# Optimization experiments

Measured on AMD Instinct MI355X. Metric: run time of the kernel, lower is better.

The kernel has to match this reference:

```python
import jax, jax.numpy as jnp
import numpy as np

EMBED = 768
N_HEADS = 12
HEAD = EMBED // N_HEADS  # 64
B, T = 2, 2048


def setup_inputs() -> dict:
    key = jax.random.key(0)
    ks = jax.random.split(key, 5)
    s = 0.02
    return {
        "x": jax.random.normal(ks[0], (B, T, EMBED), dtype=jnp.float32),
        "w_attn": jax.random.normal(ks[1], (EMBED, 3 * EMBED), dtype=jnp.float32) * s,
        "b_attn": jnp.zeros((3 * EMBED,), dtype=jnp.float32),
        "w_proj": jax.random.normal(ks[2], (EMBED, EMBED), dtype=jnp.float32) * s,
        "b_proj": jnp.zeros((EMBED,), dtype=jnp.float32),
    }


def reference(x, w_attn, b_attn, w_proj, b_proj):
    b, t, c = x.shape
    scale = HEAD ** -0.5
    qkv = x @ w_attn + b_attn  # [b,t,3c]
    q, k, v = jnp.split(qkv, 3, axis=-1)

    # einops 'b t (h n) -> b n t h' with n=N_HEADS: channel dim factors as
    # (head_size, n_heads) — head index is the inner factor.
    def split_heads(u):
        return u.reshape(b, t, HEAD, N_HEADS).transpose(0, 3, 1, 2)  # [b,n,t,h]

    q, k, v = split_heads(q), split_heads(k), split_heads(v)

    scores = jnp.einsum("bnth,bnsh->bnts", q, k) * scale  # [b,n,t,t]
    causal = jnp.tril(jnp.ones((t, t), dtype=bool))
    scores = jnp.where(causal, scores, jnp.finfo(scores.dtype).min)
    weights = jax.nn.softmax(scores, axis=-1)
    att = jnp.einsum("bnts,bnsh->bnth", weights, v)  # [b,n,t,h]

    # 'b n t h -> b t (n h)': heads are the OUTER factor on output
    att = att.transpose(0, 2, 1, 3).reshape(b, t, c)
    return att @ w_proj + b_proj
```

## Files before the change

### kernel.cpp

```cpp
#include <hip/hip_runtime.h>
#include <hip/hip_bf16.h>
#include <math.h>

#define NB      2
#define T_SZ    2048
#define EMBEDC  768
#define NHEADS  12
#define HEADD   64
#define QKV_PER (NB * NHEADS * T_SZ * HEADD)
#define QSCALE  0.18033688011112042f

typedef __bf16 bf16x8 __attribute__((ext_vector_type(8)));
typedef float  f32x4  __attribute__((ext_vector_type(4)));

__device__ inline ushort f2bf(float x) {
    union { float f; uint u; } v; v.f = x;
    uint r = v.u + 0x7fffu + ((v.u >> 16) & 1u);
    return (ushort)(r >> 16);
}

__device__ inline uint pack2bf(float a, float b) {
    union { __bf16 h[2]; uint u; } t;
    t.h[0] = (__bf16)a; t.h[1] = (__bf16)b;
    return t.u;
}

__device__ inline void gload16(const ushort* g, ushort* l) {
    __builtin_amdgcn_global_load_lds(
        (const __attribute__((address_space(1))) unsigned int*)g,
        (__attribute__((address_space(3))) unsigned int*)l, 16, 0, 0);
}

__global__ __launch_bounds__(256) void cast_k(const float* __restrict__ in,
                                              ushort* __restrict__ out, int n)
{
    int i = (blockIdx.x * 256 + threadIdx.x) * 8;
    if (i >= n) return;
    float4 a = *(const float4*)(in + i);
    float4 b = *(const float4*)(in + i + 4);
    union { ushort u[8]; int4 v; } p;
    p.u[0] = f2bf(a.x); p.u[1] = f2bf(a.y); p.u[2] = f2bf(a.z); p.u[3] = f2bf(a.w);
    p.u[4] = f2bf(b.x); p.u[5] = f2bf(b.y); p.u[6] = f2bf(b.z); p.u[7] = f2bf(b.w);
    *(int4*)(out + i) = p.v;
}

template <int PERM>
__global__ __launch_bounds__(256) void tcast_k(const float* __restrict__ in,
                                               ushort* __restrict__ out,
                                               int R, int C)
{
    __shared__ float t[32][33];
    const int c0 = blockIdx.x * 32, r0 = blockIdx.y * 32;
    const int tx = threadIdx.x & 31, ty = threadIdx.x >> 5;
#pragma unroll
    for (int u = 0; u < 4; ++u)
        t[ty + 8 * u][tx] = in[(size_t)(r0 + ty + 8 * u) * C + c0 + tx];
    __syncthreads();
#pragma unroll
    for (int u = 0; u < 4; ++u) {
        int n = c0 + ty + 8 * u;
        int orow = n;
        if (PERM) {
            int mat = n / EMBEDC, cc = n % EMBEDC;
            orow = mat * EMBEDC + (cc % NHEADS) * HEADD + cc / NHEADS;
        }
        out[(size_t)orow * R + r0 + tx] = f2bf(t[tx][ty + 8 * u]);
    }
}

__global__ __launch_bounds__(256) void vt_k(const ushort* __restrict__ in,
                                            ushort* __restrict__ out)
{
    __shared__ ushort tile[64][66];
    const int bh = blockIdx.y;
    const int t0 = blockIdx.x * 64;
    const int tid = threadIdx.x;
#pragma unroll
    for (int u = 0; u < 2; ++u) {
        int s = tid + 256 * u;
        int r = s >> 3, c8 = s & 7;
        *(bf16x8*)&tile[r][c8 * 8] =
            *(const bf16x8*)(in + ((size_t)bh * T_SZ + t0 + r) * HEADD + c8 * 8);
    }
    __syncthreads();
#pragma unroll
    for (int u = 0; u < 2; ++u) {
        int s = tid + 256 * u;
        int hd = s >> 3, tt = s & 7;
        union { ushort v[8]; int4 q; } pk;
#pragma unroll
        for (int j = 0; j < 8; ++j) pk.v[j] = tile[tt * 8 + j][hd];
        *(int4*)(out + ((size_t)bh * HEADD + hd) * T_SZ + t0 + tt * 8) = pk.q;
    }
}

#define STAGE(buf, koff)                                        \
    do {                                                        \
        gload16(gA0 + (koff), &As[buf][lA0o]);                  \
        gload16(gA1 + (koff), &As[buf][lA1o]);                  \
        gload16(gB0 + (koff), &Bs[buf][lB0o]);                  \
        gload16(gB1 + (koff), &Bs[buf][lB1o]);                  \
    } while (0)

template <int MODE>
__global__ __launch_bounds__(256) void gemm_bf16_k(
    const ushort* __restrict__ A, const ushort* __restrict__ Bt,
    const float* __restrict__ bias, void* __restrict__ outp,
    int M, int N, int K)
{
    __shared__ ushort As[2][128 * 32];
    __shared__ ushort Bs[2][128 * 32];

    const int tid = threadIdx.x;
    const int w = tid >> 6, l = tid & 63;
    const int g = l >> 4, r16 = l & 15;
    const int wr = w >> 1, wc = w & 1;
    const int m0 = blockIdx.y * 128, n0 = blockIdx.x * 128;

    const int srow = l >> 2;
    const int scol = ((l & 3) ^ (srow & 3)) * 8;
    const ushort* gA0 = A + (size_t)(m0 + 32 * w + srow) * K + scol;
    const ushort* gA1 = gA0 + (size_t)16 * K;
    const ushort* gB0 = Bt + (size_t)(n0 + 32 * w + srow) * K + scol;
    const ushort* gB1 = gB0 + (size_t)16 * K;
    const int lA0o = (32 * w) * 32,      lA1o = (32 * w + 16) * 32;
    const int lB0o = lA0o,               lB1o = lA1o;

    f32x4 acc[4][4];
#pragma unroll
    for (int i = 0; i < 4; ++i)
#pragma unroll
        for (int j = 0; j < 4; ++j) acc[i][j] = (f32x4){0.f, 0.f, 0.f, 0.f};

    const int rck = (r16 & 3);

    STAGE(0, 0);
    __syncthreads();

    int cur = 0;
    for (int k0 = 0; k0 < K; k0 += 32) {
        if (k0 + 32 < K) STAGE(cur ^ 1, k0 + 32);

        const ushort* sA = As[cur];
        const ushort* sB = Bs[cur];
        bf16x8 af[4], bfr[4];
#pragma unroll
        for (int ms = 0; ms < 4; ++ms) {
            int row = 64 * wr + 16 * ms + r16;
            af[ms] = *(const bf16x8*)&sA[row * 32 + ((g ^ rck) * 8)];
        }
#pragma unroll
        for (int ns = 0; ns < 4; ++ns) {
            int row = 64 * wc + 16 * ns + r16;
            bfr[ns] = *(const bf16x8*)&sB[row * 32 + ((g ^ rck) * 8)];
        }
#pragma unroll
        for (int ms = 0; ms < 4; ++ms)
#pragma unroll
            for (int ns = 0; ns < 4; ++ns)
                acc[ms][ns] = __builtin_amdgcn_mfma_f32_16x16x32_bf16(
                    af[ms], bfr[ns], acc[ms][ns], 0, 0, 0);

        __syncthreads();
        cur ^= 1;
    }

#pragma unroll
    for (int ns = 0; ns < 4; ++ns) {
        const int n = n0 + 64 * wc + 16 * ns + r16;
        if (MODE == 0) {
            float* out = (float*)outp;
            const float bv = bias[n];
#pragma unroll
            for (int ms = 0; ms < 4; ++ms) {
                const int mb = m0 + 64 * wr + 16 * ms + 4 * g;
#pragma unroll
                for (int r = 0; r < 4; ++r)
                    out[(size_t)(mb + r) * N + n] = acc[ms][ns][r] + bv;
            }
        } else {
            ushort* ob = (ushort*)outp;
            const int mat  = n / EMBEDC;
            const int c    = n - mat * EMBEDC;
            const int head = c >> 6;
            const int hd   = c & 63;
            const float bv = bias[mat * EMBEDC + hd * NHEADS + head];
            const float qs = (mat == 0) ? QSCALE : 1.f;
#pragma unroll
            for (int ms = 0; ms < 4; ++ms) {
                const int mb = m0 + 64 * wr + 16 * ms + 4 * g;
#pragma unroll
                for (int r = 0; r < 4; ++r) {
                    const int m = mb + r;
                    const int b = m >> 11, t = m & 2047;
                    const size_t bh = (size_t)(b * NHEADS + head);
                    ob[(size_t)mat * QKV_PER + (bh * T_SZ + t) * HEADD + hd] =
                        f2bf((acc[ms][ns][r] + bv) * qs);
                }
            }
        }
    }
}

__global__ __launch_bounds__(256, 3) void attn_mfma_k(
    const ushort* __restrict__ Qb, const ushort* __restrict__ Kb,
    const ushort* __restrict__ Vtb, ushort* __restrict__ Out)
{
    __shared__ ushort Ks[128 * 64];
    __shared__ ushort Vs[64 * 128];

    const int qb = blockIdx.x;
    const int bh = blockIdx.y;
    const int bb = bh / NHEADS, head = bh % NHEADS;
    const int tid = threadIdx.x;
    const int w = tid >> 6, l = tid & 63;
    const int g = l >> 4, r16 = l & 15;
    const int q0 = qb * 64;
    const int nt = qb / 2 + 1;
    const ushort* Kg = Qb ? Kb + (size_t)bh * T_SZ * HEADD : nullptr;
    const ushort* Vg = Vtb + (size_t)bh * HEADD * T_SZ;

    bf16x8 qf[2];
    {
        const ushort* qp = Qb + (size_t)bh * T_SZ * HEADD +
                           (size_t)(q0 + 16 * w + r16) * HEADD + g * 8;
        qf[0] = *(const bf16x8*)(qp);
        qf[1] = *(const bf16x8*)(qp + 32);
    }

    f32x4 o[4];
#pragma unroll
    for (int dc = 0; dc < 4; ++dc) o[dc] = (f32x4){0.f, 0.f, 0.f, 0.f};
    float mR = -1e30f, lR = 0.f;

    bf16x8 kr[4], vr[4];
#pragma unroll
    for (int u = 0; u < 4; ++u) {
        int s = tid + 256 * u;
        kr[u] = *(const bf16x8*)(Kg + (size_t)(s >> 3) * HEADD + (s & 7) * 8);
        vr[u] = *(const bf16x8*)(Vg + (size_t)(s >> 4) * T_SZ + (s & 15) * 8);
    }
#pragma unroll
    for (int u = 0; u < 4; ++u) {
        int s = tid + 256 * u;
        int krow = s >> 3, kc8 = s & 7;
        int vrow = s >> 4, vc16 = s & 15;
        *(bf16x8*)&Ks[krow * 64 + ((kc8 ^ (krow & 7)) * 8)] = kr[u];
        *(bf16x8*)&Vs[vrow * 128 + ((vc16 ^ (vrow & 15)) * 8)] = vr[u];
    }
    __syncthreads();

    const int srcLo = ((g & 1) << 5) | r16;
    const int srcHi = srcLo + 16;
    const bool hiSel = (g >> 1) != 0;
    const int qg = q0 + 16 * w + r16;

    for (int kt = 0; kt < nt; ++kt) {
        if (kt + 1 < nt) {
            const int k1 = (kt + 1) * 128;
#pragma unroll
            for (int u = 0; u < 4; ++u) {
                int s = tid + 256 * u;
                kr[u] = *(const bf16x8*)(Kg + (size_t)(k1 + (s >> 3)) * HEADD +
                                         (s & 7) * 8);
                vr[u] = *(const bf16x8*)(Vg + (size_t)(s >> 4) * T_SZ + k1 +
                                         (s & 15) * 8);
            }
        }

        f32x4 st[8];
#pragma unroll
        for (int kc = 0; kc < 8; ++kc) {
            int row = kc * 16 + r16;
            const ushort* krow = &Ks[row * 64];
            bf16x8 a0 = *(const bf16x8*)(krow + ((g    ) ^ (row & 7)) * 8);
            bf16x8 a1 = *(const bf16x8*)(krow + ((g + 4) ^ (row & 7)) * 8);
            f32x4 c = (f32x4){0.f, 0.f, 0.f, 0.f};
            c = __builtin_amdgcn_mfma_f32_16x16x32_bf16(a0, qf[0], c, 0, 0, 0);
            c = __builtin_amdgcn_mfma_f32_16x16x32_bf16(a1, qf[1], c, 0, 0, 0);
            st[kc] = c;
        }

        if (kt == nt - 1) {
            const int k0 = kt * 128;
#pragma unroll
            for (int kc = 0; kc < 8; ++kc)
#pragma unroll
                for (int r = 0; r < 4; ++r)
                    if (k0 + kc * 16 + 4 * g + r > qg) st[kc][r] = -1e30f;
        }

        float pm = -1e30f;
#pragma unroll
        for (int kc = 0; kc < 8; ++kc)
#pragma unroll
            for (int r = 0; r < 4; ++r) pm = fmaxf(pm, st[kc][r]);
        pm = fmaxf(pm, __shfl_xor(pm, 16));
        pm = fmaxf(pm, __shfl_xor(pm, 32));
        if (!__all(pm - mR <= 8.f)) {
            float mNew = fmaxf(mR, pm);
            float sc = exp2f(mR - mNew);
            lR *= sc;
#pragma unroll
            for (int dc = 0; dc < 4; ++dc) o[dc] *= sc;
            mR = mNew;
        }
        float rs = 0.f;
#pragma unroll
        for (int kc = 0; kc < 8; ++kc)
#pragma unroll
            for (int r = 0; r < 4; ++r) {
                float e = exp2f(st[kc][r] - mR);
                st[kc][r] = e;
                rs += e;
            }
        rs += __shfl_xor(rs, 16);
        rs += __shfl_xor(rs, 32);
        lR += rs;

        uint pk[8][2];
#pragma unroll
        for (int kc = 0; kc < 8; ++kc) {
            pk[kc][0] = pack2bf(st[kc][0], st[kc][1]);
            pk[kc][1] = pack2bf(st[kc][2], st[kc][3]);
        }

#pragma unroll
        for (int s = 0; s < 4; ++s) {
            uint A0 = (uint)__shfl((int)pk[2 * s][0],     srcLo);
            uint A1 = (uint)__shfl((int)pk[2 * s][1],     srcLo);
            uint B0 = (uint)__shfl((int)pk[2 * s + 1][0], srcLo);
            uint B1 = (uint)__shfl((int)pk[2 * s + 1][1], srcLo);
            uint A2 = (uint)__shfl((int)pk[2 * s][0],     srcHi);
            uint A3 = (uint)__shfl((int)pk[2 * s][1],     srcHi);
            uint B2 = (uint)__shfl((int)pk[2 * s + 1][0], srcHi);
            uint B3 = (uint)__shfl((int)pk[2 * s + 1][1], srcHi);
            union { uint u[4]; bf16x8 v; } t;
            t.u[0] = hiSel ? B0 : A0;
            t.u[1] = hiSel ? B1 : A1;
            t.u[2] = hiSel ? B2 : A2;
            t.u[3] = hiSel ? B3 : A3;
#pragma unroll
            for (int dc = 0; dc < 4; ++dc) {
                int row = dc * 16 + r16;
                bf16x8 vf = *(const bf16x8*)
                    &Vs[row * 128 + (((4 * s + g) ^ (row & 15)) * 8)];
                o[dc] = __builtin_amdgcn_mfma_f32_16x16x32_bf16(
                    vf, t.v, o[dc], 0, 0, 0);
            }
        }

        __syncthreads();
        if (kt + 1 < nt) {
#pragma unroll
            for (int u = 0; u < 4; ++u) {
                int s = tid + 256 * u;
                int krow = s >> 3, kc8 = s & 7;
                int vrow = s >> 4, vc16 = s & 15;
                *(bf16x8*)&Ks[krow * 64 + ((kc8 ^ (krow & 7)) * 8)] = kr[u];
                *(bf16x8*)&Vs[vrow * 128 + ((vc16 ^ (vrow & 15)) * 8)] = vr[u];
            }
            __syncthreads();
        }
    }

    const float inv = 1.f / lR;
    ushort* orow = Out + ((size_t)(bb * T_SZ + qg)) * EMBEDC + head * HEADD;
#pragma unroll
    for (int dc = 0; dc < 4; ++dc)
#pragma unroll
        for (int r = 0; r < 4; ++r)
            orow[dc * 16 + 4 * g + r] = f2bf(o[dc][r] * inv);
}

extern "C" void kernel_launch(void* const* d_in, const int* in_sizes, int n_in,
                              void* d_out, int out_size, void* d_ws, size_t ws_size,
                              hipStream_t stream)
{
    const float* x      = (const float*)d_in[0];
    const float* w_attn = (const float*)d_in[1];
    const float* b_attn = (const float*)d_in[2];
    const float* w_proj = (const float*)d_in[3];
    const float* b_proj = (const float*)d_in[4];
    float* out = (float*)d_out;

    ushort* qw   = (ushort*)d_ws;
    ushort* vT   = qw + (size_t)3 * QKV_PER;
    ushort* attb = vT + QKV_PER;
    ushort* xb   = attb + QKV_PER;
    ushort* waT  = xb + QKV_PER;
    ushort* wpT  = waT + (size_t)EMBEDC * 3 * EMBEDC;

    cast_k<<<QKV_PER / (256 * 8), 256, 0, stream>>>(x, xb, QKV_PER);
    tcast_k<1><<<dim3(3 * EMBEDC / 32, EMBEDC / 32), 256, 0, stream>>>(
        w_attn, waT, EMBEDC, 3 * EMBEDC);
    tcast_k<0><<<dim3(EMBEDC / 32, EMBEDC / 32), 256, 0, stream>>>(
        w_proj, wpT, EMBEDC, EMBEDC);

    gemm_bf16_k<1><<<dim3(2304 / 128, 4096 / 128), 256, 0, stream>>>(
        xb, waT, b_attn, qw, NB * T_SZ, 3 * EMBEDC, EMBEDC);

    vt_k<<<dim3(T_SZ / 64, NB * NHEADS), 256, 0, stream>>>(
        qw + 2 * (size_t)QKV_PER, vT);

    attn_mfma_k<<<dim3(T_SZ / 64, NB * NHEADS), 256, 0, stream>>>(
        qw, qw + QKV_PER, vT, attb);

    gemm_bf16_k<0><<<dim3(768 / 128, 4096 / 128), 256, 0, stream>>>(
        attb, wpT, b_proj, out, NB * T_SZ, EMBEDC, EMBEDC);
}
```

Before: 131.4 us.

## Split attention KV tile across warps and pair causal query blocks per workgroup

The attention kernel now has each warp process all 64 queries against its own 32-row slice of each 128-key tile, instead of each warp owning 16 queries and sweeping the whole tile. Partial softmax states and outputs are then merged across warps through shared memory. Each workgroup also handles a short and a long causal query block (qb and 31-qb), which halves the grid and balances the triangular work. The cost is more registers (occupancy bound drops from 3 to 2 blocks), extra reduction passes with several barriers, and more LDS.

```diff
diff --git a/kernel.cpp b/kernel.cpp
--- a/kernel.cpp
+++ b/kernel.cpp
@@ -202,175 +202,279 @@
     }
 }
 
-__global__ __launch_bounds__(256, 3) void attn_mfma_k(
+__global__ __launch_bounds__(256, 2) void attn_mfma_k(
     const ushort* __restrict__ Qb, const ushort* __restrict__ Kb,
     const ushort* __restrict__ Vtb, ushort* __restrict__ Out)
 {
-    __shared__ ushort Ks[128 * 64];
-    __shared__ ushort Vs[64 * 128];
-
-    const int qb = blockIdx.x;
+    __shared__ ushort smem[16384];
+    __shared__ float Ml[4 * 64], Ll[4 * 64];
+
+    ushort* Ks = smem;
+    ushort* Vs = smem + 8192;
+
+    const int pairIdx = blockIdx.x;
     const int bh = blockIdx.y;
     const int bb = bh / NHEADS, head = bh % NHEADS;
     const int tid = threadIdx.x;
     const int w = tid >> 6, l = tid & 63;
     const int g = l >> 4, r16 = l & 15;
-    const int q0 = qb * 64;
-    const int nt = qb / 2 + 1;
-    const ushort* Kg = Qb ? Kb + (size_t)bh * T_SZ * HEADD : nullptr;
+    const ushort* Qg = Qb + (size_t)bh * T_SZ * HEADD;
+    const ushort* Kg = Kb + (size_t)bh * T_SZ * HEADD;
     const ushort* Vg = Vtb + (size_t)bh * HEADD * T_SZ;
-
-    bf16x8 qf[2];
-    {
-        const ushort* qp = Qb + (size_t)bh * T_SZ * HEADD +
-                           (size_t)(q0 + 16 * w + r16) * HEADD + g * 8;
-        qf[0] = *(const bf16x8*)(qp);
-        qf[1] = *(const bf16x8*)(qp + 32);
-    }
-
-    f32x4 o[4];
-#pragma unroll
-    for (int dc = 0; dc < 4; ++dc) o[dc] = (f32x4){0.f, 0.f, 0.f, 0.f};
-    float mR = -1e30f, lR = 0.f;
-
-    bf16x8 kr[4], vr[4];
-#pragma unroll
-    for (int u = 0; u < 4; ++u) {
-        int s = tid + 256 * u;
-        kr[u] = *(const bf16x8*)(Kg + (size_t)(s >> 3) * HEADD + (s & 7) * 8);
-        vr[u] = *(const bf16x8*)(Vg + (size_t)(s >> 4) * T_SZ + (s & 15) * 8);
-    }
-#pragma unroll
-    for (int u = 0; u < 4; ++u) {
-        int s = tid + 256 * u;
-        int krow = s >> 3, kc8 = s & 7;
-        int vrow = s >> 4, vc16 = s & 15;
-        *(bf16x8*)&Ks[krow * 64 + ((kc8 ^ (krow & 7)) * 8)] = kr[u];
-        *(bf16x8*)&Vs[vrow * 128 + ((vc16 ^ (vrow & 15)) * 8)] = vr[u];
-    }
-    __syncthreads();
 
     const int srcLo = ((g & 1) << 5) | r16;
     const int srcHi = srcLo + 16;
-    const bool hiSel = (g >> 1) != 0;
-    const int qg = q0 + 16 * w + r16;
-
-    for (int kt = 0; kt < nt; ++kt) {
-        if (kt + 1 < nt) {
-            const int k1 = (kt + 1) * 128;
-#pragma unroll
-            for (int u = 0; u < 4; ++u) {
-                int s = tid + 256 * u;
-                kr[u] = *(const bf16x8*)(Kg + (size_t)(k1 + (s >> 3)) * HEADD +
-                                         (s & 7) * 8);
-                vr[u] = *(const bf16x8*)(Vg + (size_t)(s >> 4) * T_SZ + k1 +
-                                         (s & 15) * 8);
-            }
-        }
-
-        f32x4 st[8];
-#pragma unroll
-        for (int kc = 0; kc < 8; ++kc) {
-            int row = kc * 16 + r16;
-            const ushort* krow = &Ks[row * 64];
-            bf16x8 a0 = *(const bf16x8*)(krow + ((g    ) ^ (row & 7)) * 8);
-            bf16x8 a1 = *(const bf16x8*)(krow + ((g + 4) ^ (row & 7)) * 8);
-            f32x4 c = (f32x4){0.f, 0.f, 0.f, 0.f};
-            c = __builtin_amdgcn_mfma_f32_16x16x32_bf16(a0, qf[0], c, 0, 0, 0);
-            c = __builtin_amdgcn_mfma_f32_16x16x32_bf16(a1, qf[1], c, 0, 0, 0);
-            st[kc] = c;
-        }
-
-        if (kt == nt - 1) {
-            const int k0 = kt * 128;
-#pragma unroll
-            for (int kc = 0; kc < 8; ++kc)
-#pragma unroll
-                for (int r = 0; r < 4; ++r)
-                    if (k0 + kc * 16 + 4 * g + r > qg) st[kc][r] = -1e30f;
-        }
-
-        float pm = -1e30f;
-#pragma unroll
-        for (int kc = 0; kc < 8; ++kc)
-#pragma unroll
-            for (int r = 0; r < 4; ++r) pm = fmaxf(pm, st[kc][r]);
-        pm = fmaxf(pm, __shfl_xor(pm, 16));
-        pm = fmaxf(pm, __shfl_xor(pm, 32));
-        if (!__all(pm - mR <= 8.f)) {
-            float mNew = fmaxf(mR, pm);
-            float sc = exp2f(mR - mNew);
-            lR *= sc;
-#pragma unroll
-            for (int dc = 0; dc < 4; ++dc) o[dc] *= sc;
-            mR = mNew;
-        }
-        float rs = 0.f;
-#pragma unroll
-        for (int kc = 0; kc < 8; ++kc)
-#pragma unroll
-            for (int r = 0; r < 4; ++r) {
-                float e = exp2f(st[kc][r] - mR);
-                st[kc][r] = e;
-                rs += e;
-            }
-        rs += __shfl_xor(rs, 16);
-        rs += __shfl_xor(rs, 32);
-        lR += rs;
-
-        uint pk[8][2];
-#pragma unroll
-        for (int kc = 0; kc < 8; ++kc) {
-            pk[kc][0] = pack2bf(st[kc][0], st[kc][1]);
-            pk[kc][1] = pack2bf(st[kc][2], st[kc][3]);
-        }
-
-#pragma unroll
-        for (int s = 0; s < 4; ++s) {
-            uint A0 = (uint)__shfl((int)pk[2 * s][0],     srcLo);
-            uint A1 = (uint)__shfl((int)pk[2 * s][1],     srcLo);
-            uint B0 = (uint)__shfl((int)pk[2 * s + 1][0], srcLo);
-            uint B1 = (uint)__shfl((int)pk[2 * s + 1][1], srcLo);
-            uint A2 = (uint)__shfl((int)pk[2 * s][0],     srcHi);
-            uint A3 = (uint)__shfl((int)pk[2 * s][1],     srcHi);
-            uint B2 = (uint)__shfl((int)pk[2 * s + 1][0], srcHi);
-            uint B3 = (uint)__shfl((int)pk[2 * s + 1][1], srcHi);
-            union { uint u[4]; bf16x8 v; } t;
-            t.u[0] = hiSel ? B0 : A0;
-            t.u[1] = hiSel ? B1 : A1;
-            t.u[2] = hiSel ? B2 : A2;
-            t.u[3] = hiSel ? B3 : A3;
+    const bool kcSel = (g >> 1) != 0;
+
+    for (int rep = 0; rep < 2; ++rep) {
+        const int qb = rep ? (31 - pairIdx) : pairIdx;
+        const int q0 = qb * 64;
+        const int nt = qb / 2 + 1;
+
+        bf16x8 qf[4][2];
+#pragma unroll
+        for (int qi = 0; qi < 4; ++qi) {
+            const ushort* qp = Qg + (size_t)(q0 + qi * 16 + r16) * HEADD + g * 8;
+            qf[qi][0] = *(const bf16x8*)(qp);
+            qf[qi][1] = *(const bf16x8*)(qp + 32);
+        }
+
+        f32x4 o[4][4];
+#pragma unroll
+        for (int dc = 0; dc < 4; ++dc)
+#pragma unroll
+            for (int qi = 0; qi < 4; ++qi) o[dc][qi] = (f32x4){0.f,0.f,0.f,0.f};
+        float mR[4], lR[4];
+#pragma unroll
+        for (int qi = 0; qi < 4; ++qi) { mR[qi] = -1e30f; lR[qi] = 0.f; }
+
+        __syncthreads();
+
+        bf16x8 kr[4], vr[4];
+#pragma unroll
+        for (int u = 0; u < 4; ++u) {
+            int s = tid + 256 * u;
+            kr[u] = *(const bf16x8*)(Kg + (size_t)(s >> 3) * HEADD + (s & 7) * 8);
+            vr[u] = *(const bf16x8*)(Vg + (size_t)(s >> 4) * T_SZ + (s & 15) * 8);
+        }
+#pragma unroll
+        for (int u = 0; u < 4; ++u) {
+            int s = tid + 256 * u;
+            int krow = s >> 3, kc8 = s & 7;
+            int vrow = s >> 4, vc16 = s & 15;
+            *(bf16x8*)&Ks[krow * 64 + ((kc8 ^ (krow & 7)) * 8)] = kr[u];
+            *(bf16x8*)&Vs[vrow * 128 + ((vc16 ^ (vrow & 15)) * 8)] = vr[u];
+        }
+        __syncthreads();
+
+        for (int kt = 0; kt < nt; ++kt) {
+            if (kt + 1 < nt) {
+                const int k1 = (kt + 1) * 128;
+#pragma unroll
+                for (int u = 0; u < 4; ++u) {
+                    int s = tid + 256 * u;
+                    kr[u] = *(const bf16x8*)(Kg + (size_t)(k1 + (s >> 3)) * HEADD +
+                                             (s & 7) * 8);
+                    vr[u] = *(const bf16x8*)(Vg + (size_t)(s >> 4) * T_SZ + k1 +
+                                             (s & 15) * 8);
+                }
+            }
+
+            f32x4 st[2][4];
+#pragma unroll
+            for (int kc = 0; kc < 2; ++kc) {
+                int row = 32 * w + kc * 16 + r16;
+                const ushort* kp = &Ks[row * 64];
+                bf16x8 a0 = *(const bf16x8*)(kp + ((g    ) ^ (r16 & 7)) * 8);
+                bf16x8 a1 = *(const bf16x8*)(kp + ((g + 4) ^ (r16 & 7)) * 8);
+#pragma unroll
+                for (int qi = 0; qi < 4; ++qi) {
+                    f32x4 c = (f32x4){0.f, 0.f, 0.f, 0.f};
+                    c = __builtin_amdgcn_mfma_f32_16x16x32_bf16(a0, qf[qi][0], c, 0, 0, 0);
+                    c = __builtin_amdgcn_mfma_f32_16x16x32_bf16(a1, qf[qi][1], c, 0, 0, 0);
+                    st[kc][qi] = c;
+                }
+            }
+
+            if (kt == nt - 1) {
+                const int kvb = kt * 128 + 32 * w;
+#pragma unroll
+                for (int kc = 0; kc < 2; ++kc)
+#pragma unroll
+                    for (int qi = 0; qi < 4; ++qi)
+#pragma unroll
+                        for (int r = 0; r < 4; ++r)
+                            if (kvb + kc * 16 + 4 * g + r > q0 + qi * 16 + r16)
+                                st[kc][qi][r] = -1e30f;
+            }
+
+            float pm[4];
+#pragma unroll
+            for (int qi = 0; qi < 4; ++qi) {
+                float m = fmaxf(fmaxf(st[0][qi][0], st[0][qi][1]),
+                                fmaxf(st[0][qi][2], st[0][qi][3]));
+                m = fmaxf(m, fmaxf(fmaxf(st[1][qi][0], st[1][qi][1]),
+                                   fmaxf(st[1][qi][2], st[1][qi][3])));
+                m = fmaxf(m, __shfl_xor(m, 16));
+                m = fmaxf(m, __shfl_xor(m, 32));
+                pm[qi] = m;
+            }
+            float dm = fmaxf(fmaxf(pm[0] - mR[0], pm[1] - mR[1]),
+                             fmaxf(pm[2] - mR[2], pm[3] - mR[3]));
+            if (!__all(dm <= 8.f)) {
+#pragma unroll
+                for (int qi = 0; qi < 4; ++qi) {
+                    float mNew = fmaxf(mR[qi], pm[qi]);
+                    float sc = exp2f(mR[qi] - mNew);
+                    lR[qi] *= sc;
+                    mR[qi] = mNew;
+#pragma unroll
+                    for (int dc = 0; dc < 4; ++dc) o[dc][qi] *= sc;
+                }
+            }
+#pragma unroll
+            for (int qi = 0; qi < 4; ++qi) {
+                float rs = 0.f;
+#pragma unroll
+                for (int kc = 0; kc < 2; ++kc)
+#pragma unroll
+                    for (int r = 0; r < 4; ++r) {
+                        float e = exp2f(st[kc][qi][r] - mR[qi]);
+                        st[kc][qi][r] = e;
+                        rs += e;
+                    }
+                rs += __shfl_xor(rs, 16);
+                rs += __shfl_xor(rs, 32);
+                lR[qi] += rs;
+            }
+
+            uint pk[4][2][2];
+#pragma unroll
+            for (int qi = 0; qi < 4; ++qi)
+#pragma unroll
+                for (int kc = 0; kc < 2; ++kc) {
+                    pk[qi][kc][0] = pack2bf(st[kc][qi][0], st[kc][qi][1]);
+                    pk[qi][kc][1] = pack2bf(st[kc][qi][2], st[kc][qi][3]);
+                }
+
+            bf16x8 vf[4];
 #pragma unroll
             for (int dc = 0; dc < 4; ++dc) {
                 int row = dc * 16 + r16;
-                bf16x8 vf = *(const bf16x8*)
-                    &Vs[row * 128 + (((4 * s + g) ^ (row & 15)) * 8)];
-                o[dc] = __builtin_amdgcn_mfma_f32_16x16x32_bf16(
-                    vf, t.v, o[dc], 0, 0, 0);
-            }
-        }
-
-        __syncthreads();
-        if (kt + 1 < nt) {
-#pragma unroll
-            for (int u = 0; u < 4; ++u) {
-                int s = tid + 256 * u;
-                int krow = s >> 3, kc8 = s & 7;
-                int vrow = s >> 4, vc16 = s & 15;
-                *(bf16x8*)&Ks[krow * 64 + ((kc8 ^ (krow & 7)) * 8)] = kr[u];
-                *(bf16x8*)&Vs[vrow * 128 + ((vc16 ^ (vrow & 15)) * 8)] = vr[u];
-            }
+                vf[dc] = *(const bf16x8*)
+                    &Vs[row * 128 + (((4 * w + g) ^ (row & 15)) * 8)];
+            }
+
+#pragma unroll
+            for (int qi = 0; qi < 4; ++qi) {
+                uint A0 = (uint)__shfl((int)pk[qi][0][0], srcLo);
+                uint A1 = (uint)__shfl((int)pk[qi][0][1], srcLo);
+                uint B0 = (uint)__shfl((int)pk[qi][1][0], srcLo);
+                uint B1 = (uint)__shfl((int)pk[qi][1][1], srcLo);
+                uint A2 = (uint)__shfl((int)pk[qi][0][0], srcHi);
+                uint A3 = (uint)__shfl((int)pk[qi][0][1], srcHi);
+                uint B2 = (uint)__shfl((int)pk[qi][1][0], srcHi);
+                uint B3 = (uint)__shfl((int)pk[qi][1][1], srcHi);
+                union { uint u[4]; bf16x8 v; } t;
+                t.u[0] = kcSel ? B0 : A0;
+                t.u[1] = kcSel ? B1 : A1;
+                t.u[2] = kcSel ? B2 : A2;
+                t.u[3] = kcSel ? B3 : A3;
+#pragma unroll
+                for (int dc = 0; dc < 4; ++dc)
+                    o[dc][qi] = __builtin_amdgcn_mfma_f32_16x16x32_bf16(
+                        vf[dc], t.v, o[dc][qi], 0, 0, 0);
+            }
+
             __syncthreads();
+            if (kt + 1 < nt) {
+#pragma unroll
+                for (int u = 0; u < 4; ++u) {
+                    int s = tid + 256 * u;
+                    int krow = s >> 3, kc8 = s & 7;
+                    int vrow = s >> 4, vc16 = s & 15;
+                    *(bf16x8*)&Ks[krow * 64 + ((kc8 ^ (krow & 7)) * 8)] = kr[u];
+                    *(bf16x8*)&Vs[vrow * 128 + ((vc16 ^ (vrow & 15)) * 8)] = vr[u];
+                }
+                __syncthreads();
+            }
+        }
+
+        if (g == 0) {
+#pragma unroll
+            for (int qi = 0; qi < 4; ++qi) {
+                Ml[w * 64 + qi * 16 + r16] = mR[qi];
+                Ll[w * 64 + qi * 16 + r16] = lR[qi];
+            }
+        }
+        __syncthreads();
+
+        float lt[4];
+#pragma unroll
+        for (int qi = 0; qi < 4; ++qi) {
+            const int ix = qi * 16 + r16;
+            float m0 = Ml[ix], m1 = Ml[64 + ix], m2 = Ml[128 + ix], m3 = Ml[192 + ix];
+            float mt = fmaxf(fmaxf(m0, m1), fmaxf(m2, m3));
+            float f = exp2f(mR[qi] - mt);
+#pragma unroll
+            for (int dc = 0; dc < 4; ++dc) o[dc][qi] *= f;
+            lt[qi] = Ll[ix]       * exp2f(m0 - mt) + Ll[64 + ix]  * exp2f(m1 - mt)
+                   + Ll[128 + ix] * exp2f(m2 - mt) + Ll[192 + ix] * exp2f(m3 - mt);
+        }
+        __syncthreads();
+
+        float* img0 = (float*)smem;
+        float* img1 = (float*)smem + 4096;
+
+        if (w >= 2) {
+            float* img = (w == 2) ? img0 : img1;
+#pragma unroll
+            for (int dc = 0; dc < 4; ++dc)
+#pragma unroll
+                for (int qi = 0; qi < 4; ++qi)
+#pragma unroll
+                    for (int r = 0; r < 4; ++r)
+                        img[(dc * 16 + 4 * g + r) * 64 + qi * 16 + r16] = o[dc][qi][r];
+        }
+        __syncthreads();
+        if (w < 2) {
+            const float* img = (w == 0) ? img0 : img1;
+#pragma unroll
+            for (int dc = 0; dc < 4; ++dc)
+#pragma unroll
+                for (int qi = 0; qi < 4; ++qi)
+#pragma unroll
+                    for (int r = 0; r < 4; ++r)
+                        o[dc][qi][r] += img[(dc * 16 + 4 * g + r) * 64 + qi * 16 + r16];
+        }
+        __syncthreads();
+        if (w == 1) {
+#pragma unroll
+            for (int dc = 0; dc < 4; ++dc)
+#pragma unroll
+                for (int qi = 0; qi < 4; ++qi)
+#pragma unroll
+                    for (int r = 0; r < 4; ++r)
+                        img0[(dc * 16 + 4 * g + r) * 64 + qi * 16 + r16] = o[dc][qi][r];
+        }
+        __syncthreads();
+        if (w == 0) {
+#pragma unroll
+            for (int qi = 0; qi < 4; ++qi) {
+                const float inv = 1.f / lt[qi];
+                ushort* orow = Out + ((size_t)(bb * T_SZ + q0 + qi * 16 + r16)) * EMBEDC
+                             + head * HEADD;
+#pragma unroll
+                for (int dc = 0; dc < 4; ++dc)
+#pragma unroll
+                    for (int r = 0; r < 4; ++r) {
+                        float v = o[dc][qi][r] +
+                            img0[(dc * 16 + 4 * g + r) * 64 + qi * 16 + r16];
+                        orow[dc * 16 + 4 * g + r] = f2bf(v * inv);
+                    }
+            }
         }
     }
-
-    const float inv = 1.f / lR;
-    ushort* orow = Out + ((size_t)(bb * T_SZ + qg)) * EMBEDC + head * HEADD;
-#pragma unroll
-    for (int dc = 0; dc < 4; ++dc)
-#pragma unroll
-        for (int r = 0; r < 4; ++r)
-            orow[dc * 16 + 4 * g + r] = f2bf(o[dc][r] * inv);
 }
 
 extern "C" void kernel_launch(void* const* d_in, const int* in_sizes, int n_in,
@@ -403,7 +507,7 @@
     vt_k<<<dim3(T_SZ / 64, NB * NHEADS), 256, 0, stream>>>(
         qw + 2 * (size_t)QKV_PER, vT);
 
-    attn_mfma_k<<<dim3(T_SZ / 64, NB * NHEADS), 256, 0, stream>>>(
+    attn_mfma_k<<<dim3(16, NB * NHEADS), 256, 0, stream>>>(
         qw, qw + QKV_PER, vT, attb);
 
     gemm_bf16_k<0><<<dim3(768 / 128, 4096 / 128), 256, 0, stream>>>(
```

New measurement: 131.9 us. Within noise of the previous version (+0.4%).

## Rewrite attention as single-wave 32x32 MFMA kernel with causal pairing

Applied to the files above, without the earlier changes.

Replaces the 256-thread attention block, which staged K and V through LDS, with a 64-thread single-wave kernel. Each wave reads K and V straight from global memory into registers and uses 32x32x16 MFMA tiles. Each block handles a pair of query tiles (p and 63-p) to balance causal work, and block IDs are mapped so heads are grouped per XCD for L2 locality. This removes LDS traffic and __syncthreads, but relies on cache hits for the repeated global K/V reads and gives less latency hiding per wave.

```diff
diff --git a/kernel.cpp b/kernel.cpp
--- a/kernel.cpp
+++ b/kernel.cpp
@@ -12,6 +12,7 @@
 
 typedef __bf16 bf16x8 __attribute__((ext_vector_type(8)));
 typedef float  f32x4  __attribute__((ext_vector_type(4)));
+typedef float  f32x16 __attribute__((ext_vector_type(16)));
 
 __device__ inline ushort f2bf(float x) {
     union { float f; uint u; } v; v.f = x;
@@ -202,175 +203,134 @@
     }
 }
 
-__global__ __launch_bounds__(256, 3) void attn_mfma_k(
+__global__ __launch_bounds__(64) void attn_mfma_k(
     const ushort* __restrict__ Qb, const ushort* __restrict__ Kb,
     const ushort* __restrict__ Vtb, ushort* __restrict__ Out)
 {
-    __shared__ ushort Ks[128 * 64];
-    __shared__ ushort Vs[64 * 128];
-
-    const int qb = blockIdx.x;
-    const int bh = blockIdx.y;
+    const int bid = blockIdx.x;
+    const int xcd = bid & 7, jj = bid >> 3;
+    const int bh = xcd * 3 + (jj >> 5);
+    const int p  = jj & 31;
     const int bb = bh / NHEADS, head = bh % NHEADS;
-    const int tid = threadIdx.x;
-    const int w = tid >> 6, l = tid & 63;
-    const int g = l >> 4, r16 = l & 15;
-    const int q0 = qb * 64;
-    const int nt = qb / 2 + 1;
-    const ushort* Kg = Qb ? Kb + (size_t)bh * T_SZ * HEADD : nullptr;
+    const int l = threadIdx.x;
+    const int q31 = l & 31, hi = l >> 5;
+    const ushort* Qg = Qb + (size_t)bh * T_SZ * HEADD;
+    const ushort* Kg = Kb + (size_t)bh * T_SZ * HEADD;
     const ushort* Vg = Vtb + (size_t)bh * HEADD * T_SZ;
 
-    bf16x8 qf[2];
-    {
-        const ushort* qp = Qb + (size_t)bh * T_SZ * HEADD +
-                           (size_t)(q0 + 16 * w + r16) * HEADD + g * 8;
-        qf[0] = *(const bf16x8*)(qp);
-        qf[1] = *(const bf16x8*)(qp + 32);
-    }
-
-    f32x4 o[4];
-#pragma unroll
-    for (int dc = 0; dc < 4; ++dc) o[dc] = (f32x4){0.f, 0.f, 0.f, 0.f};
-    float mR = -1e30f, lR = 0.f;
-
-    bf16x8 kr[4], vr[4];
-#pragma unroll
-    for (int u = 0; u < 4; ++u) {
-        int s = tid + 256 * u;
-        kr[u] = *(const bf16x8*)(Kg + (size_t)(s >> 3) * HEADD + (s & 7) * 8);
-        vr[u] = *(const bf16x8*)(Vg + (size_t)(s >> 4) * T_SZ + (s & 15) * 8);
-    }
-#pragma unroll
-    for (int u = 0; u < 4; ++u) {
-        int s = tid + 256 * u;
-        int krow = s >> 3, kc8 = s & 7;
-        int vrow = s >> 4, vc16 = s & 15;
-        *(bf16x8*)&Ks[krow * 64 + ((kc8 ^ (krow & 7)) * 8)] = kr[u];
-        *(bf16x8*)&Vs[vrow * 128 + ((vc16 ^ (vrow & 15)) * 8)] = vr[u];
-    }
-    __syncthreads();
-
-    const int srcLo = ((g & 1) << 5) | r16;
-    const int srcHi = srcLo + 16;
-    const bool hiSel = (g >> 1) != 0;
-    const int qg = q0 + 16 * w + r16;
-
-    for (int kt = 0; kt < nt; ++kt) {
-        if (kt + 1 < nt) {
-            const int k1 = (kt + 1) * 128;
-#pragma unroll
-            for (int u = 0; u < 4; ++u) {
-                int s = tid + 256 * u;
-                kr[u] = *(const bf16x8*)(Kg + (size_t)(k1 + (s >> 3)) * HEADD +
-                                         (s & 7) * 8);
-                vr[u] = *(const bf16x8*)(Vg + (size_t)(s >> 4) * T_SZ + k1 +
-                                         (s & 15) * 8);
-            }
-        }
-
-        f32x4 st[8];
-#pragma unroll
-        for (int kc = 0; kc < 8; ++kc) {
-            int row = kc * 16 + r16;
-            const ushort* krow = &Ks[row * 64];
-            bf16x8 a0 = *(const bf16x8*)(krow + ((g    ) ^ (row & 7)) * 8);
-            bf16x8 a1 = *(const bf16x8*)(krow + ((g + 4) ^ (row & 7)) * 8);
-            f32x4 c = (f32x4){0.f, 0.f, 0.f, 0.f};
-            c = __builtin_amdgcn_mfma_f32_16x16x32_bf16(a0, qf[0], c, 0, 0, 0);
-            c = __builtin_amdgcn_mfma_f32_16x16x32_bf16(a1, qf[1], c, 0, 0, 0);
-            st[kc] = c;
-        }
-
-        if (kt == nt - 1) {
-            const int k0 = kt * 128;
-#pragma unroll
-            for (int kc = 0; kc < 8; ++kc)
-#pragma unroll
-                for (int r = 0; r < 4; ++r)
-                    if (k0 + kc * 16 + 4 * g + r > qg) st[kc][r] = -1e30f;
-        }
-
-        float pm = -1e30f;
-#pragma unroll
-        for (int kc = 0; kc < 8; ++kc)
-#pragma unroll
-            for (int r = 0; r < 4; ++r) pm = fmaxf(pm, st[kc][r]);
-        pm = fmaxf(pm, __shfl_xor(pm, 16));
-        pm = fmaxf(pm, __shfl_xor(pm, 32));
-        if (!__all(pm - mR <= 8.f)) {
-            float mNew = fmaxf(mR, pm);
-            float sc = exp2f(mR - mNew);
-            lR *= sc;
-#pragma unroll
-            for (int dc = 0; dc < 4; ++dc) o[dc] *= sc;
-            mR = mNew;
-        }
-        float rs = 0.f;
-#pragma unroll
-        for (int kc = 0; kc < 8; ++kc)
-#pragma unroll
-            for (int r = 0; r < 4; ++r) {
-                float e = exp2f(st[kc][r] - mR);
-                st[kc][r] = e;
+    const ushort* V0 = Vg + (size_t)q31 * T_SZ + 8 * hi;
+    const ushort* V1 = Vg + (size_t)(32 + q31) * T_SZ + 8 * hi;
+
+    for (int rep = 0; rep < 2; ++rep) {
+        const int iq = rep ? (63 - p) : p;
+        const int q0 = iq * 32;
+        const int nt = iq + 1;
+
+        const ushort* qrow = Qg + (size_t)(q0 + q31) * HEADD + 8 * hi;
+        const bf16x8 qf0 = *(const bf16x8*)(qrow);
+        const bf16x8 qf1 = *(const bf16x8*)(qrow + 16);
+        const bf16x8 qf2 = *(const bf16x8*)(qrow + 32);
+        const bf16x8 qf3 = *(const bf16x8*)(qrow + 48);
+
+        f32x16 o0, o1, z;
+#pragma unroll
+        for (int r = 0; r < 16; ++r) { o0[r] = 0.f; o1[r] = 0.f; z[r] = 0.f; }
+        float mR = -1e30f, lR = 0.f;
+
+        const ushort* Krow = Kg + (size_t)q31 * HEADD + 8 * hi;
+        bf16x8 kf0 = *(const bf16x8*)(Krow);
+        bf16x8 kf1 = *(const bf16x8*)(Krow + 16);
+        bf16x8 kf2 = *(const bf16x8*)(Krow + 32);
+        bf16x8 kf3 = *(const bf16x8*)(Krow + 48);
+
+        for (int kt = 0; kt < nt; ++kt) {
+            const int kvb = kt * 32;
+            const bf16x8 va0 = *(const bf16x8*)(V0 + kvb);
+            const bf16x8 va1 = *(const bf16x8*)(V0 + kvb + 16);
+            const bf16x8 vb0 = *(const bf16x8*)(V1 + kvb);
+            const bf16x8 vb1 = *(const bf16x8*)(V1 + kvb + 16);
+            bf16x8 kn0, kn1, kn2, kn3;
+            if (kt + 1 < nt) {
+                const ushort* kr = Krow + (size_t)(kvb + 32) * HEADD;
+                kn0 = *(const bf16x8*)(kr);
+                kn1 = *(const bf16x8*)(kr + 16);
+                kn2 = *(const bf16x8*)(kr + 32);
+                kn3 = *(const bf16x8*)(kr + 48);
+            }
+
+            f32x16 st = z;
+            st = __builtin_amdgcn_mfma_f32_32x32x16_bf16(kf0, qf0, st, 0, 0, 0);
+            st = __builtin_amdgcn_mfma_f32_32x32x16_bf16(kf1, qf1, st, 0, 0, 0);
+            st = __builtin_amdgcn_mfma_f32_32x32x16_bf16(kf2, qf2, st, 0, 0, 0);
+            st = __builtin_amdgcn_mfma_f32_32x32x16_bf16(kf3, qf3, st, 0, 0, 0);
+
+            if (kt == nt - 1) {
+#pragma unroll
+                for (int r = 0; r < 16; ++r)
+                    if (((r & 3) + 8 * (r >> 2) + 4 * hi) > q31)
+                        st[r] = -1e30f;
+            }
+
+            float pm = st[0];
+#pragma unroll
+            for (int r = 1; r < 16; ++r) pm = fmaxf(pm, st[r]);
+            pm = fmaxf(pm, __shfl_xor(pm, 32));
+            if (!__all(pm - mR <= 8.f)) {
+                float mNew = fmaxf(mR, pm);
+                float sc = exp2f(mR - mNew);
+                lR *= sc;
+                o0 *= sc;
+                o1 *= sc;
+                mR = mNew;
+            }
+            float rs = 0.f;
+#pragma unroll
+            for (int r = 0; r < 16; ++r) {
+                float e = exp2f(st[r] - mR);
+                st[r] = e;
                 rs += e;
             }
-        rs += __shfl_xor(rs, 16);
-        rs += __shfl_xor(rs, 32);
-        lR += rs;
-
-        uint pk[8][2];
-#pragma unroll
-        for (int kc = 0; kc < 8; ++kc) {
-            pk[kc][0] = pack2bf(st[kc][0], st[kc][1]);
-            pk[kc][1] = pack2bf(st[kc][2], st[kc][3]);
-        }
-
-#pragma unroll
-        for (int s = 0; s < 4; ++s) {
-            uint A0 = (uint)__shfl((int)pk[2 * s][0],     srcLo);
-            uint A1 = (uint)__shfl((int)pk[2 * s][1],     srcLo);
-            uint B0 = (uint)__shfl((int)pk[2 * s + 1][0], srcLo);
-            uint B1 = (uint)__shfl((int)pk[2 * s + 1][1], srcLo);
-            uint A2 = (uint)__shfl((int)pk[2 * s][0],     srcHi);
-            uint A3 = (uint)__shfl((int)pk[2 * s][1],     srcHi);
-            uint B2 = (uint)__shfl((int)pk[2 * s + 1][0], srcHi);
-            uint B3 = (uint)__shfl((int)pk[2 * s + 1][1], srcHi);
-            union { uint u[4]; bf16x8 v; } t;
-            t.u[0] = hiSel ? B0 : A0;
-            t.u[1] = hiSel ? B1 : A1;
-            t.u[2] = hiSel ? B2 : A2;
-            t.u[3] = hiSel ? B3 : A3;
-#pragma unroll
-            for (int dc = 0; dc < 4; ++dc) {
-                int row = dc * 16 + r16;
-                bf16x8 vf = *(const bf16x8*)
-                    &Vs[row * 128 + (((4 * s + g) ^ (row & 15)) * 8)];
-                o[dc] = __builtin_amdgcn_mfma_f32_16x16x32_bf16(
-                    vf, t.v, o[dc], 0, 0, 0);
-            }
-        }
-
-        __syncthreads();
-        if (kt + 1 < nt) {
-#pragma unroll
-            for (int u = 0; u < 4; ++u) {
-                int s = tid + 256 * u;
-                int krow = s >> 3, kc8 = s & 7;
-                int vrow = s >> 4, vc16 = s & 15;
-                *(bf16x8*)&Ks[krow * 64 + ((kc8 ^ (krow & 7)) * 8)] = kr[u];
-                *(bf16x8*)&Vs[vrow * 128 + ((vc16 ^ (vrow & 15)) * 8)] = vr[u];
-            }
-            __syncthreads();
-        }
-    }
-
-    const float inv = 1.f / lR;
-    ushort* orow = Out + ((size_t)(bb * T_SZ + qg)) * EMBEDC + head * HEADD;
-#pragma unroll
-    for (int dc = 0; dc < 4; ++dc)
-#pragma unroll
-        for (int r = 0; r < 4; ++r)
-            orow[dc * 16 + 4 * g + r] = f2bf(o[dc][r] * inv);
+            rs += __shfl_xor(rs, 32);
+            lR += rs;
+
+            uint w0 = pack2bf(st[0],  st[1]),  w1 = pack2bf(st[2],  st[3]);
+            uint w2 = pack2bf(st[4],  st[5]),  w3 = pack2bf(st[6],  st[7]);
+            uint w4 = pack2bf(st[8],  st[9]),  w5 = pack2bf(st[10], st[11]);
+            uint w6 = pack2bf(st[12], st[13]), w7 = pack2bf(st[14], st[15]);
+
+            uint e0 = (uint)__shfl_xor((int)(hi ? w0 : w2), 32);
+            uint e1 = (uint)__shfl_xor((int)(hi ? w1 : w3), 32);
+            uint e2 = (uint)__shfl_xor((int)(hi ? w4 : w6), 32);
+            uint e3 = (uint)__shfl_xor((int)(hi ? w5 : w7), 32);
+
+            union { uint u[4]; bf16x8 v; } b0, b1;
+            b0.u[0] = hi ? e0 : w0;  b0.u[1] = hi ? e1 : w1;
+            b0.u[2] = hi ? w2 : e0;  b0.u[3] = hi ? w3 : e1;
+            b1.u[0] = hi ? e2 : w4;  b1.u[1] = hi ? e3 : w5;
+            b1.u[2] = hi ? w6 : e2;  b1.u[3] = hi ? w7 : e3;
+
+            o0 = __builtin_amdgcn_mfma_f32_32x32x16_bf16(va0, b0.v, o0, 0, 0, 0);
+            o0 = __builtin_amdgcn_mfma_f32_32x32x16_bf16(va1, b1.v, o0, 0, 0, 0);
+            o1 = __builtin_amdgcn_mfma_f32_32x32x16_bf16(vb0, b0.v, o1, 0, 0, 0);
+            o1 = __builtin_amdgcn_mfma_f32_32x32x16_bf16(vb1, b1.v, o1, 0, 0, 0);
+
+            kf0 = kn0; kf1 = kn1; kf2 = kn2; kf3 = kn3;
+        }
+
+        const float inv = 1.f / lR;
+        ushort* orow = Out + ((size_t)(bb * T_SZ + q0 + q31)) * EMBEDC
+                     + head * HEADD + 4 * hi;
+#pragma unroll
+        for (int c = 0; c < 4; ++c) {
+            uint2 pv0, pv1;
+            pv0.x = pack2bf(o0[4 * c + 0] * inv, o0[4 * c + 1] * inv);
+            pv0.y = pack2bf(o0[4 * c + 2] * inv, o0[4 * c + 3] * inv);
+            pv1.x = pack2bf(o1[4 * c + 0] * inv, o1[4 * c + 1] * inv);
+            pv1.y = pack2bf(o1[4 * c + 2] * inv, o1[4 * c + 3] * inv);
+            *(uint2*)(orow + 8 * c)      = pv0;
+            *(uint2*)(orow + 32 + 8 * c) = pv1;
+        }
+    }
 }
 
 extern "C" void kernel_launch(void* const* d_in, const int* in_sizes, int n_in,
@@ -403,7 +363,7 @@
     vt_k<<<dim3(T_SZ / 64, NB * NHEADS), 256, 0, stream>>>(
         qw + 2 * (size_t)QKV_PER, vT);
 
-    attn_mfma_k<<<dim3(T_SZ / 64, NB * NHEADS), 256, 0, stream>>>(
+    attn_mfma_k<<<768, 64, 0, stream>>>(
         qw, qw + QKV_PER, vT, attb);
 
     gemm_bf16_k<0><<<dim3(768 / 128, 4096 / 128), 256, 0, stream>>>(
```

Result: no change. 132.2 us (+0.6%).
